# Kernel optimization log

Hardware: AMD Instinct MI355X
Metric: run time of the kernel (lower is better)

Reference implementation:

```python
import jax, jax.numpy as jnp
import numpy as np

B = 1024      # batch
V = 5023      # FLAME vertices
NF = 9976     # FLAME faces
NJ = 5        # joints: global, neck, jaw, eyeL, eyeR
NL = 51       # static landmarks
PARENTS = (-1, 0, 1, 1, 1)


def setup_inputs() -> dict:
    key = jax.random.key(0)
    ks = jax.random.split(key, 16)
    inp = {}
    # trainable flame parameters (small pose magnitudes for realism)
    inp['shape_params'] = jax.random.normal(ks[0], (B, 300), jnp.float32)
    inp['expression_params'] = jax.random.normal(ks[1], (B, 100), jnp.float32)
    inp['global_rot'] = 0.1 * jax.random.normal(ks[2], (B, 3), jnp.float32)
    inp['neck_pose'] = 0.1 * jax.random.normal(ks[3], (B, 3), jnp.float32)
    inp['jaw_pose'] = 0.1 * jax.random.normal(ks[4], (B, 3), jnp.float32)
    inp['eye_pose'] = 0.1 * jax.random.normal(ks[5], (B, 6), jnp.float32)
    inp['transl'] = jax.random.normal(ks[6], (B, 3), jnp.float32)
    # flame buffers
    inp['v_template'] = jax.random.normal(ks[7], (V, 3), jnp.float32)
    inp['shapedirs'] = 0.01 * jax.random.normal(ks[8], (V, 3, 400), jnp.float32)
    inp['posedirs'] = 0.01 * jax.random.normal(ks[9], (36, V * 3), jnp.float32)
    Jreg = jax.random.uniform(ks[10], (NJ, V), jnp.float32)
    inp['J_regressor'] = Jreg / jnp.sum(Jreg, axis=1, keepdims=True)
    W = jax.random.uniform(ks[11], (V, NJ), jnp.float32)
    inp['lbs_weights'] = W / jnp.sum(W, axis=1, keepdims=True)
    bc = jax.random.uniform(ks[12], (NL, 3), jnp.float32)
    inp['lmk_bary_coords'] = bc / jnp.sum(bc, axis=1, keepdims=True)
    inp['parents'] = jnp.array(PARENTS, dtype=jnp.int32)
    inp['faces'] = jax.random.randint(ks[13], (NF, 3), 0, V, jnp.int32)
    inp['lmk_faces_idx'] = jax.random.randint(ks[14], (NL,), 0, NF, jnp.int64)
    return inp


def batch_rodrigues(rvecs):
    # rvecs: [N,3] axis-angle -> [N,3,3] rotation matrices
    angle = jnp.sqrt(jnp.sum(jnp.square(rvecs + 1e-8), axis=1, keepdims=True))  # [N,1]
    axis = rvecs / angle
    s = jnp.sin(angle)[:, :, None]
    c = jnp.cos(angle)[:, :, None]
    rx, ry, rz = axis[:, 0], axis[:, 1], axis[:, 2]
    zeros = jnp.zeros_like(rx)
    K = jnp.stack([zeros, -rz, ry, rz, zeros, -rx, -ry, rx, zeros], axis=1).reshape(-1, 3, 3)
    I = jnp.eye(3, dtype=rvecs.dtype)
    return I + s * K + (1.0 - c) * (K @ K)


def _lbs(betas, full_pose, v_template, shapedirs, posedirs, J_regressor, lbs_weights):
    b = betas.shape[0]
    # shape+expression blendshapes
    v_shaped = v_template[None] + jnp.einsum('bl,vkl->bvk', betas, shapedirs)  # [B,V,3]
    joints = jnp.einsum('jv,bvk->bjk', J_regressor, v_shaped)                 # [B,J,3]
    rot_mats = batch_rodrigues(full_pose.reshape(-1, 3)).reshape(b, NJ, 3, 3)
    # pose blendshapes (exclude root)
    ident = jnp.eye(3, dtype=betas.dtype)
    pose_feature = (rot_mats[:, 1:] - ident).reshape(b, 9 * (NJ - 1))         # [B,36]
    v_posed = v_shaped + (pose_feature @ posedirs).reshape(b, V, 3)
    # rigid kinematic chain
    rel_joints = jnp.concatenate(
        [joints[:, :1], joints[:, 1:] - joints[:, jnp.array(PARENTS[1:])]], axis=1)
    bottom = jnp.broadcast_to(jnp.array([0., 0., 0., 1.], betas.dtype), (b, NJ, 1, 4))
    tf = jnp.concatenate(
        [jnp.concatenate([rot_mats, rel_joints[..., None]], axis=3), bottom], axis=2)  # [B,J,4,4]
    chain = [tf[:, 0]]
    for i in range(1, NJ):
        chain.append(chain[PARENTS[i]] @ tf[:, i])
    transforms = jnp.stack(chain, axis=1)                                    # [B,J,4,4]
    # remove rest-pose joint location from translation column
    jh = jnp.einsum('bjmn,bjn->bjm', transforms[:, :, :3, :3], joints)       # [B,J,3]
    A = transforms.at[:, :, :3, 3].add(-jh)
    # skinning
    T = jnp.einsum('vj,bjmn->bvmn', lbs_weights, A)                          # [B,V,4,4]
    v_h = jnp.concatenate([v_posed, jnp.ones((b, V, 1), betas.dtype)], axis=2)
    verts = jnp.einsum('bvmn,bvn->bvm', T, v_h)[..., :3]                     # [B,V,3]
    return verts, transforms[:, :, :3, 3]


def reference(shape_params, expression_params, global_rot, neck_pose, jaw_pose,
              eye_pose, transl, v_template, shapedirs, posedirs, J_regressor,
              lbs_weights, lmk_bary_coords, parents, faces, lmk_faces_idx):
    betas = jnp.concatenate([shape_params, expression_params], axis=1)       # [B,400]
    full_pose = jnp.concatenate([global_rot, neck_pose, jaw_pose, eye_pose], axis=1)  # [B,15]
    vertices, _ = _lbs(betas, full_pose, v_template, shapedirs, posedirs,
                       J_regressor, lbs_weights)
    # barycentric landmark interpolation
    lmk_faces = faces[lmk_faces_idx]                                         # [L,3]
    lmk_verts = vertices[:, lmk_faces]                                       # [B,L,3,3]
    landmarks_3d = jnp.einsum('blfk,lf->blk', lmk_verts, lmk_bary_coords)    # [B,L,3]
    landmarks_3d = landmarks_3d + transl[:, None]
    vertices = vertices + transl[:, None]
    # default-weights flame regularizer (fixed_shape=None, ref_vertices=None)
    flame_reg = (100.0 * jnp.sum(neck_pose ** 2)
                 + 0.001 * jnp.sum(jaw_pose ** 2)
                 + 0.001 * jnp.sum(shape_params ** 2)
                 + 0.001 * jnp.sum(expression_params ** 2))
    return vertices, landmarks_3d, flame_reg
```

## Files before the change

### kernel.cpp

```cpp
#include <hip/hip_runtime.h>
#include <hip/hip_bf16.h>

#define BATCH 1024
#define NV 5023
#define NJOINT 5
#define NLMK 51
#define N3 (NV*3)
#define NPADB 15072
#define KBETA 400
#define KTOT 448
#define NSTEP 14
#define RB_B (NPADB/16)
#define RB_A 64
#define FRAG 512

#define BM 64
#define BN 48

#define PK_BETA_CH (NPADB*50)
#define PK_BETA_BLKS 2944
#define PK_POSE_CH (RB_B*96)
#define PK_POSE_BLKS 354
#define NVC2 360
#define VCH 14
#define PK_JS_BLKS (3*NVC2)

#define GBM 64
#define GBN 192
#define GNP 79
#define GGRID 1280
#define CH_S 52
#define CH_PAD 4

typedef __attribute__((ext_vector_type(8))) short short8;
typedef __attribute__((ext_vector_type(4))) float floatx4;
typedef __attribute__((ext_vector_type(4))) float float4v;

#define GLDS16(gp, lp) \
    __builtin_amdgcn_global_load_lds( \
        (const __attribute__((address_space(1))) void*)(gp), \
        (__attribute__((address_space(3))) void*)(lp), 16, 0, 0)

#define WS_JS      0
#define WS_BASEJ   24064
#define WS_REG     24512
#define WS_FLAGS   24520
#define WS_AMAT    24576
#define WS_ACT     270336
#define WS_WB      1187840
#define WS_FULL    14692352

__device__ __forceinline__ float ldf(const void* p, long i, int f32) {
    if (f32) return ((const float*)p)[i];
    return __bfloat162float(((const __hip_bfloat16*)p)[i]);
}
__device__ __forceinline__ short8 ld8bf(const void* p, long i, int f32) {
    if (f32) {
        float4v a = *(const float4v*)((const float*)p + i);
        float4v b = *(const float4v*)((const float*)p + i + 4);
        short8 r;
#pragma unroll
        for (int j = 0; j < 4; ++j) {
            __hip_bfloat16 h = __float2bfloat16(a[j]);
            r[j] = *reinterpret_cast<short*>(&h);
        }
#pragma unroll
        for (int j = 0; j < 4; ++j) {
            __hip_bfloat16 h = __float2bfloat16(b[j]);
            r[4 + j] = *reinterpret_cast<short*>(&h);
        }
        return r;
    }
    return *(const short8*)((const __hip_bfloat16*)p + i);
}
__device__ __forceinline__ void stf(void* p, long i, float v, int f32) {
    if (f32) ((float*)p)[i] = v;
    else ((__hip_bfloat16*)p)[i] = __float2bfloat16(v);
}

__device__ __forceinline__ long act2_off(int b, int k) {
    return (((long)(k >> 5) * RB_A + (b >> 4)) * 64 + ((k >> 3) & 3) * 16 + (b & 15)) * 8 + (k & 7);
}

__device__ __forceinline__ int probe_f32(const void* shape_p) {
    int lane = threadIdx.x & 63;
    unsigned short h = ((const unsigned short*)shape_p)[2 * lane];
    union { unsigned short u; __hip_bfloat16 b; } cv; cv.u = h;
    float v = fabsf(__bfloat162float(cv.b));
    if (v != v) v = 3.4e38f;
#pragma unroll
    for (int off = 32; off; off >>= 1) v = fmaxf(v, __shfl_down(v, off));
    v = __shfl(v, 0);
    return v > 1e4f;
}
__device__ __forceinline__ int probe_i64(const void* lmk_idx) {
    int lane = threadIdx.x & 63;
    const int* q = (const int*)lmk_idx;
    int odd_nonzero = (lane < 25) && (q[2*lane + 1] != 0);
    unsigned long long b = __ballot(odd_nonzero);
    return b == 0ull;
}

__global__ void k_init(float* ws0, const void* shape_p, const void* lmk_idx, int* flags) {
    int i = blockIdx.x * 256 + threadIdx.x;
    if (i < 6129) ws0[i] = 0.f;
    if (blockIdx.x == 0 && threadIdx.x < 64) {
        int f = probe_f32(shape_p);
        int i64 = probe_i64(lmk_idx);
        if (threadIdx.x == 0) { flags[0] = f; flags[1] = i64; }
    }
}

__global__ __launch_bounds__(256) void k_prep(const void* __restrict__ shapedirs,
                                              const void* __restrict__ posedirs,
                                              const void* __restrict__ Jreg,
                                              const void* __restrict__ v_template,
                                              const void* __restrict__ shape_p,
                                              float* __restrict__ reg,
                                              float* __restrict__ JS,
                                              float* __restrict__ baseJ,
                                              __hip_bfloat16* __restrict__ Wb,
                                              float* __restrict__ PART) {
    __shared__ float jl[NJOINT * VCH];
    int f32 = probe_f32(shape_p);
    int blk = blockIdx.x, tid = threadIdx.x;
    if (blk < PK_BETA_BLKS) {
        if (blk == 0 && tid == 0) reg[0] = 0.f;
        if (blk < 24) {
            int zi = blk * 256 + tid;
            if (zi < 6000) JS[zi] = 0.f;
            if (zi < 15) baseJ[zi] = 0.f;
        }
        int g = blk * 256 + tid;
        if (g >= PK_BETA_CH) return;
        int n = g / 50, kg = g - n * 50;
        short8 o;
#pragma unroll
        for (int e = 0; e < 8; ++e) o[e] = 0;
        if (n < N3) o = ld8bf(shapedirs, (long)n * KBETA + kg * 8, f32);
        long chunk = ((long)(kg >> 2) * RB_B + (n >> 4)) * 64 + (kg & 3) * 16 + (n & 15);
        *(short8*)(Wb + chunk * 8) = o;
    } else if (blk < PK_BETA_BLKS + PK_POSE_BLKS) {
        int g = (blk - PK_BETA_BLKS) * 256 + tid;
        if (g >= PK_POSE_CH) return;
        int R = g / 96, rem = g - R * 96;
        int c = rem >> 4, fr = rem & 15;
        int n = R * 16 + fr;
        int k0 = KBETA + 8 * c;
        short8 o;
#pragma unroll
        for (int e = 0; e < 8; ++e) o[e] = 0;
        if (n < N3) {
#pragma unroll
            for (int e = 0; e < 8; ++e) {
                int kk = k0 + e - KBETA;
                float val = (kk < 36) ? ldf(posedirs, (long)kk * N3 + n, f32) : 0.f;
                __hip_bfloat16 h = __float2bfloat16(val);
                o[e] = *reinterpret_cast<short*>(&h);
            }
        }
        long chunk = ((long)(k0 >> 5) * RB_B + R) * 64 + ((k0 >> 3) & 3) * 16 + fr;
        *(short8*)(Wb + chunk * 8) = o;
    } else {
        int b2 = blk - (PK_BETA_BLKS + PK_POSE_BLKS);
        int k = b2 / NVC2;
        int vc = b2 - k * NVC2;
        int v0 = vc * VCH;
        if (tid < NJOINT * VCH) {
            int j = tid / VCH, i = tid - j * VCH;
            int v = min(v0 + i, NV - 1);
            jl[tid] = ldf(Jreg, (long)j * NV + v, f32);
        }
        __syncthreads();
        int l2 = tid + 256;
        float acc1[NJOINT] = {0,0,0,0,0};
        float acc2[NJOINT] = {0,0,0,0,0};
#pragma unroll
        for (int i = 0; i < VCH; ++i) {
            int v = v0 + i;
            if (v >= NV) break;
            float s1 = ldf(shapedirs, (long)v*1200 + k*400 + tid, f32);
            float s2 = 0.f;
            if (l2 < 400)       s2 = ldf(shapedirs, (long)v*1200 + k*400 + l2, f32);
            else if (l2 == 400) s2 = ldf(v_template, v*3 + k, f32);
#pragma unroll
            for (int j = 0; j < NJOINT; ++j) {
                float jr = jl[j*VCH + i];
                acc1[j] += jr * s1;
                acc2[j] += jr * s2;
            }
        }
        long base = ((long)(k*NVC2 + vc)*5)*401;
#pragma unroll
        for (int j = 0; j < NJOINT; ++j) {
            PART[base + j*401 + tid] = acc1[j];
            if (l2 <= 400) PART[base + j*401 + l2] = acc2[j];
        }
    }
}

__global__ __launch_bounds__(256) void k_js_red(const float* __restrict__ PART,
                                                float* __restrict__ JS,
                                                float* __restrict__ baseJ) {
    int o = blockIdx.x * 256 + threadIdx.x;
    if (o >= 3*5*401) return;
    int g = blockIdx.y;
    int k = o / 2005, r = o - k*2005;
    int j = r / 401, l = r - j*401;
    float s = 0.f;
    long base = ((long)(k*NVC2 + g*60)*5 + j)*401 + l;
    for (int vc = 0; vc < 60; ++vc) s += PART[base + (long)vc*2005];
    if (l < 400) atomicAdd(&JS[j*1200 + k*400 + l], s);
    else         atomicAdd(&baseJ[j*3 + k], s);
}

__global__ void k_js_atomic(const void* __restrict__ Jreg,
                            const void* __restrict__ shapedirs,
                            const void* __restrict__ v_template,
                            const int* __restrict__ flags,
                            float* __restrict__ JS, float* __restrict__ baseJ) {
    int f32 = flags[0];
    int k = blockIdx.x, vc = blockIdx.y, tid = threadIdx.x;
    int v0 = vc * 79, v1 = min(NV, v0 + 79);
    int l2 = tid + 256;
    float acc1[NJOINT] = {0,0,0,0,0};
    float acc2[NJOINT] = {0,0,0,0,0};
    for (int v = v0; v < v1; ++v) {
        float s1 = ldf(shapedirs, (long)v*1200 + k*400 + tid, f32);
        float s2 = 0.f;
        if (l2 < 400)       s2 = ldf(shapedirs, (long)v*1200 + k*400 + l2, f32);
        else if (l2 == 400) s2 = ldf(v_template, v*3 + k, f32);
#pragma unroll
        for (int j = 0; j < NJOINT; ++j) {
            float jr = ldf(Jreg, j*NV + v, f32);
            acc1[j] += jr * s1;
            acc2[j] += jr * s2;
        }
    }
#pragma unroll
    for (int j = 0; j < NJOINT; ++j) {
        atomicAdd(&JS[j*1200 + k*400 + tid], acc1[j]);
        if (l2 < 400)       atomicAdd(&JS[j*1200 + k*400 + l2], acc2[j]);
        else if (l2 == 400) atomicAdd(&baseJ[j*3 + k], acc2[j]);
    }
}

__global__ __launch_bounds__(64) void k_batch(
        const void* __restrict__ shape_p, const void* __restrict__ expr_p,
        const void* __restrict__ grot, const void* __restrict__ neck,
        const void* __restrict__ jaw,  const void* __restrict__ eye,
        const float* __restrict__ JS, const float* __restrict__ baseJ,
        __hip_bfloat16* __restrict__ Act, float* __restrict__ Amat, float* __restrict__ reg) {
    int f32 = probe_f32(shape_p);
    int b = blockIdx.x, tid = threadIdx.x;
    __shared__ float betas[400];
    __shared__ float Rm[NJOINT][9];
    __shared__ float joints[NJOINT][3];
    __shared__ float Gm[NJOINT][12];

    for (int i = tid; i < 400; i += 64) {
        float v = (i < 300) ? ldf(shape_p, b*300 + i, f32)
                            : ldf(expr_p, b*100 + i - 300, f32);
        betas[i] = v;
        Act[act2_off(b, i)] = __float2bfloat16(v);
    }
    if (tid >= 36 && tid < 48) Act[act2_off(b, 400 + tid)] = __float2bfloat16(0.f);
    __syncthreads();

    if (tid < 60) {
        int o = tid % 15, q = tid / 15;
        int j = o / 3, kk = o - 3*j;
        const float* js = &JS[j*1200 + kk*400 + q*100];
        float s = 0.f;
        for (int l = 0; l < 100; ++l) s += js[l] * betas[q*100 + l];
        s += __shfl_down(s, 15);
        s += __shfl_down(s, 30);
        if (q == 0) joints[j][kk] = s + baseJ[o];
    }
    if (tid < NJOINT) {
        int j = tid;
        float r[3];
        for (int c = 0; c < 3; ++c) {
            if (j == 0)      r[c] = ldf(grot, b*3 + c, f32);
            else if (j == 1) r[c] = ldf(neck, b*3 + c, f32);
            else if (j == 2) r[c] = ldf(jaw,  b*3 + c, f32);
            else if (j == 3) r[c] = ldf(eye,  b*6 + c, f32);
            else             r[c] = ldf(eye,  b*6 + 3 + c, f32);
        }
        float a0 = r[0] + 1e-8f, a1 = r[1] + 1e-8f, a2 = r[2] + 1e-8f;
        float angle = sqrtf(a0*a0 + a1*a1 + a2*a2);
        float inv = 1.0f / angle;
        float rx = r[0]*inv, ry = r[1]*inv, rz = r[2]*inv;
        float s = sinf(angle), c = cosf(angle);
        float K[9] = {0.f, -rz, ry,  rz, 0.f, -rx,  -ry, rx, 0.f};
        float K2[9];
        for (int rr = 0; rr < 3; ++rr)
            for (int cc = 0; cc < 3; ++cc) {
                float t = 0.f;
                for (int m = 0; m < 3; ++m) t += K[rr*3+m] * K[m*3+cc];
                K2[rr*3+cc] = t;
            }
        for (int i2 = 0; i2 < 9; ++i2) {
            float id = (i2 == 0 || i2 == 4 || i2 == 8) ? 1.f : 0.f;
            Rm[j][i2] = id + s*K[i2] + (1.f - c)*K2[i2];
        }
    }
    __syncthreads();

    if (tid < 36) {
        int i = tid / 9 + 1, rc = tid - (tid/9)*9;
        float id = (rc == 0 || rc == 4 || rc == 8) ? 1.f : 0.f;
        Act[act2_off(b, 400 + tid)] = __float2bfloat16(Rm[i][rc] - id);
    }
    if (tid == 0) {
        for (int rr = 0; rr < 3; ++rr) {
            for (int cc = 0; cc < 3; ++cc) Gm[0][rr*4+cc] = Rm[0][rr*3+cc];
            Gm[0][rr*4+3] = joints[0][rr];
        }
        const int par[NJOINT] = {-1, 0, 1, 1, 1};
        for (int j = 1; j < NJOINT; ++j) {
            int p = par[j];
            float rel[3];
            for (int c2 = 0; c2 < 3; ++c2) rel[c2] = joints[j][c2] - joints[p][c2];
            for (int rr = 0; rr < 3; ++rr) {
                for (int cc = 0; cc < 3; ++cc) {
                    float t = 0.f;
                    for (int m = 0; m < 3; ++m) t += Gm[p][rr*4+m] * Rm[j][m*3+cc];
                    Gm[j][rr*4+cc] = t;
                }
                float t = Gm[p][rr*4+3];
                for (int m = 0; m < 3; ++m) t += Gm[p][rr*4+m] * rel[m];
                Gm[j][rr*4+3] = t;
            }
        }
    }
    __syncthreads();

    if (tid < 60) {
        int j = tid / 12, e = tid - j*12, rr = e / 4, cc = e - rr*4;
        float val = Gm[j][e];
        if (cc == 3)
            for (int m = 0; m < 3; ++m) val -= Gm[j][rr*4+m] * joints[j][m];
        Amat[b*60 + tid] = val;
    }

    float part = 0.f;
    for (int i = tid; i < 400; i += 64) part += betas[i]*betas[i];
    part *= 0.001f;
    if (tid == 0) {
        float nn = 0.f, jj = 0.f;
        for (int c = 0; c < 3; ++c) {
            float nv = ldf(neck, b*3+c, f32);
            float jv = ldf(jaw,  b*3+c, f32);
            nn += nv*nv; jj += jv*jv;
        }
        part += 100.f*nn + 0.001f*jj;
    }
    for (int off = 32; off; off >>= 1) part += __shfl_down(part, off);
    if (tid == 0) atomicAdd(reg, part);
}

__global__ __launch_bounds__(512, 2) void k_gemm_lbs_big(
        const __hip_bfloat16* __restrict__ Act,
        const __hip_bfloat16* __restrict__ Wb,
        const void* __restrict__ v_template,
        const float* __restrict__ Amat,
        const void* __restrict__ weights,
        const void* __restrict__ transl,
        const void* __restrict__ shape_p,
        void* __restrict__ out) {
    __shared__ __align__(16) __hip_bfloat16 stage[2][16 * FRAG];
    __shared__ float chunk[8][16 * CH_S + CH_PAD];
    __shared__ float Al[GBM * 60];
    __shared__ float wl[64 * 5];
    __shared__ float tl[GBM * 3];
    __shared__ float vtl[GBN];

    int f32 = probe_f32(shape_p);
    int tid = threadIdx.x;
    int wave = tid >> 6, lane = tid & 63;
    int fr = lane & 15, quad = lane >> 4;
    int mg = wave >> 2, wn = wave & 3;

    int lin = blockIdx.x;
    int xcd = lin & 7, slot = lin >> 3;
    int P = (slot >> 4) * 8 + xcd;
    int mblk = slot & 15;
    if (P >= GNP) return;
    int m0 = mblk * GBM;
    int v0 = P * 64;

    for (int i = tid; i < GBM*60/4; i += 512)
        ((float4v*)Al)[i] = ((const float4v*)(Amat + (long)m0*60))[i];
    if (tid < 320) {
        int v = v0 + tid / 5;
        wl[tid] = (v < NV) ? ldf(weights, v*5 + tid % 5, f32) : 0.f;
    }
    if (tid < GBM*3)
        tl[tid] = ldf(transl, (long)m0*3 + tid, f32);
    if (tid >= 320) {
        int i = tid - 320;
        vtl[i] = ((long)v0*3 + i < N3) ? ldf(v_template, (long)v0*3 + i, f32) : 0.f;
    }

    int r0 = wave*2, r1 = wave*2 + 1;
    long aoff0 = 0, aoff1 = 0;
    const __hip_bfloat16* base0;
    const __hip_bfloat16* base1;
    int sstr0, sstr1;
    {
        if (r0 < 4) { base0 = Act; sstr0 = RB_A; aoff0 = mblk*4 + r0; }
        else {
            long rb = (long)P*12 + (r0 - 4);
            if (rb > RB_B-1) rb = RB_B-1;
            base0 = Wb; sstr0 = RB_B; aoff0 = rb;
        }
        if (r1 < 4) { base1 = Act; sstr1 = RB_A; aoff1 = mblk*4 + r1; }
        else {
            long rb = (long)P*12 + (r1 - 4);
            if (rb > RB_B-1) rb = RB_B-1;
            base1 = Wb; sstr1 = RB_B; aoff1 = rb;
        }
    }
    __hip_bfloat16* lds0[2] = { &stage[0][r0*FRAG], &stage[1][r0*FRAG] };
    __hip_bfloat16* lds1[2] = { &stage[0][r1*FRAG], &stage[1][r1*FRAG] };

    floatx4 acc[2][3];
#pragma unroll
    for (int q = 0; q < 2; ++q)
#pragma unroll
        for (int t = 0; t < 3; ++t) acc[q][t] = (floatx4){0.f,0.f,0.f,0.f};

    asm volatile("s_waitcnt vmcnt(0)" ::: "memory");
    __builtin_amdgcn_sched_barrier(0);
    GLDS16(base0 + ((long)0*sstr0 + aoff0)*FRAG + lane*8, lds0[0]);
    GLDS16(base1 + ((long)0*sstr1 + aoff1)*FRAG + lane*8, lds1[0]);
    GLDS16(base0 + ((long)1*sstr0 + aoff0)*FRAG + lane*8, lds0[1]);
    GLDS16(base1 + ((long)1*sstr1 + aoff1)*FRAG + lane*8, lds1[1]);

#pragma unroll
    for (int s = 0; s < NSTEP; ++s) {
        const int cb = s & 1;
        if (s == NSTEP-1) { asm volatile("s_waitcnt vmcnt(0)" ::: "memory"); }
        else              { asm volatile("s_waitcnt vmcnt(2)" ::: "memory"); }
        __builtin_amdgcn_sched_barrier(0);
        __builtin_amdgcn_s_barrier();
        __builtin_amdgcn_sched_barrier(0);
        const __hip_bfloat16* sb = stage[cb];
        short8 a0 = *(const short8*)&sb[(mg*2 + 0)*FRAG + lane*8];
        short8 a1 = *(const short8*)&sb[(mg*2 + 1)*FRAG + lane*8];
        short8 b0 = *(const short8*)&sb[(4 + wn*3 + 0)*FRAG + lane*8];
        short8 b1 = *(const short8*)&sb[(4 + wn*3 + 1)*FRAG + lane*8];
        short8 b2 = *(const short8*)&sb[(4 + wn*3 + 2)*FRAG + lane*8];
        acc[0][0] = __builtin_amdgcn_mfma_f32_16x16x32_bf16(a0, b0, acc[0][0], 0, 0, 0);
        acc[0][1] = __builtin_amdgcn_mfma_f32_16x16x32_bf16(a0, b1, acc[0][1], 0, 0, 0);
        acc[0][2] = __builtin_amdgcn_mfma_f32_16x16x32_bf16(a0, b2, acc[0][2], 0, 0, 0);
        acc[1][0] = __builtin_amdgcn_mfma_f32_16x16x32_bf16(a1, b0, acc[1][0], 0, 0, 0);
        acc[1][1] = __builtin_amdgcn_mfma_f32_16x16x32_bf16(a1, b1, acc[1][1], 0, 0, 0);
        acc[1][2] = __builtin_amdgcn_mfma_f32_16x16x32_bf16(a1, b2, acc[1][2], 0, 0, 0);
        __builtin_amdgcn_sched_barrier(0);
        __builtin_amdgcn_s_barrier();
        __builtin_amdgcn_sched_barrier(0);
        if (s + 2 < NSTEP) {
            GLDS16(base0 + ((long)(s+2)*sstr0 + aoff0)*FRAG + lane*8, lds0[cb]);
            GLDS16(base1 + ((long)(s+2)*sstr1 + aoff1)*FRAG + lane*8, lds1[cb]);
        }
    }

    __syncthreads();
    float* vbuf = (float*)stage;
    float* ch = chunk[wave];
    int mloc_w = lane;
    float w0 = wl[mloc_w*5+0], w1 = wl[mloc_w*5+1], w2 = wl[mloc_w*5+2];
    float w3 = wl[mloc_w*5+3], w4 = wl[mloc_w*5+4];
    float vt0 = vtl[mloc_w*3+0], vt1 = vtl[mloc_w*3+1], vt2 = vtl[mloc_w*3+2];
    int coff = (mloc_w & 15) * 3;
    int wnl = mloc_w >> 4;
#pragma unroll
    for (int q = 0; q < 2; ++q) {
#pragma unroll
        for (int t = 0; t < 3; ++t)
#pragma unroll
            for (int rr = 0; rr < 4; ++rr)
                ch[(quad*4 + rr)*CH_S + t*16 + fr] = acc[q][t][rr];
        __syncthreads();
        int v = v0 + mloc_w;
#pragma unroll
        for (int it = 0; it < 4; ++it) {
            int r32 = it*8 + wave;
            int mb = ((r32 & 16) << 1) + q*16 + (r32 & 15);
            const float* A = &Al[mb*60];
            const float* cc2 = &chunk[((r32 >> 4) << 2) + wnl][(r32 & 15)*CH_S + coff];
            if (v < NV) {
                float p0 = cc2[0] + vt0;
                float p1 = cc2[1] + vt1;
                float p2 = cc2[2] + vt2;
                float* vb = &vbuf[r32*192 + mloc_w*3];
#pragma unroll
                for (int c = 0; c < 3; ++c) {
                    float t0 = w0*A[c*4+0] + w1*A[12+c*4+0] + w2*A[24+c*4+0] + w3*A[36+c*4+0] + w4*A[48+c*4+0];
                    float t1 = w0*A[c*4+1] + w1*A[12+c*4+1] + w2*A[24+c*4+1] + w3*A[36+c*4+1] + w4*A[48+c*4+1];
                    float t2 = w0*A[c*4+2] + w1*A[12+c*4+2] + w2*A[24+c*4+2] + w3*A[36+c*4+2] + w4*A[48+c*4+2];
                    float t3 = w0*A[c*4+3] + w1*A[12+c*4+3] + w2*A[24+c*4+3] + w3*A[36+c*4+3] + w4*A[48+c*4+3];
                    vb[c] = t0*p0 + t1*p1 + t2*p2 + t3 + tl[mb*3+c];
                }
            }
        }
        __syncthreads();
#pragma unroll
        for (int it = 0; it < 12; ++it) {
            int idx = it*512 + tid;
            int r32 = idx / 192;
            int col = idx - r32*192;
            if (v0*3 + col < N3) {
                int mb = ((r32 & 16) << 1) + q*16 + (r32 & 15);
                stf(out, ((long)(m0 + mb)*NV + v0)*3 + col, vbuf[idx], f32);
            }
        }
        __syncthreads();
    }
}

__global__ __launch_bounds__(256) void k_gemm_lbs_small(
        const __hip_bfloat16* __restrict__ Act,
        const void* __restrict__ shapedirs,
        const void* __restrict__ posedirs,
        const void* __restrict__ v_template,
        const float* __restrict__ Amat,
        const void* __restrict__ weights,
        const void* __restrict__ transl,
        const int* __restrict__ flags,
        void* __restrict__ out) {
    __shared__ float tileS[4][16*49 + 4];
    __shared__ float AlS[4][960];
    __shared__ float wl[80];
    __shared__ __align__(16) __hip_bfloat16 Bs2[BN * 64];

    int f32 = flags[0];
    int tid = threadIdx.x;
    int wave = tid >> 6, lane = tid & 63;
    int fr = lane & 15, quad = lane >> 4;
    int m0 = blockIdx.x * 256;
    int n0 = blockIdx.y * BN;
    int v0 = blockIdx.y * 16;

    if (tid < 80) {
        int v = v0 + tid / 5;
        wl[tid] = (v < NV) ? ldf(weights, v*5 + tid % 5, f32) : 0.f;
    }
    for (int i = tid; i < BN * 64; i += 256) {
        int n = i >> 6, kk = i & 63;
        int nc = min(n0 + n, N3 - 1);
        float val = 0.f;
        if (kk < 16)      val = ldf(shapedirs, (long)nc*KBETA + 384 + kk, f32);
        else if (kk < 52) val = ldf(posedirs, (long)(kk-16)*N3 + nc, f32);
        Bs2[n*64 + kk] = __float2bfloat16(val);
    }
    __syncthreads();

    int Ra0 = (m0 >> 4) + wave*4;
    int nr[3];
#pragma unroll
    for (int t = 0; t < 3; ++t) nr[t] = min(n0 + t*16 + fr, N3 - 1);

    floatx4 acc[4][3];
#pragma unroll
    for (int sub = 0; sub < 4; ++sub)
#pragma unroll
        for (int t = 0; t < 3; ++t) acc[sub][t] = (floatx4){0.f,0.f,0.f,0.f};

#pragma unroll
    for (int s = 0; s < 14; ++s) {
        short8 bb[3];
#pragma unroll
        for (int t = 0; t < 3; ++t) {
            if (s < 12) bb[t] = ld8bf(shapedirs, (long)nr[t]*KBETA + s*32 + quad*8, f32);
            else        bb[t] = *(short8*)&Bs2[(t*16 + fr)*64 + (s-12)*32 + quad*8];
        }
#pragma unroll
        for (int sub = 0; sub < 4; ++sub) {
            short8 a = *(const short8*)(Act + (((long)s*RB_A + Ra0 + sub)*64 + lane)*8);
#pragma unroll
            for (int t = 0; t < 3; ++t)
                acc[sub][t] = __builtin_amdgcn_mfma_f32_16x16x32_bf16(a, bb[t], acc[sub][t], 0, 0, 0);
        }
    }

    int vloc = fr, rgrp = quad;
    int v = v0 + vloc;
    float tpl0 = 0.f, tpl1 = 0.f, tpl2 = 0.f;
    if (v < NV) {
        tpl0 = ldf(v_template, v*3 + 0, f32);
        tpl1 = ldf(v_template, v*3 + 1, f32);
        tpl2 = ldf(v_template, v*3 + 2, f32);
    }
    float w0 = wl[vloc*5+0], w1 = wl[vloc*5+1], w2 = wl[vloc*5+2];
    float w3 = wl[vloc*5+3], w4 = wl[vloc*5+4];
    for (int sub = 0; sub < 4; ++sub) {
#pragma unroll
        for (int t = 0; t < 3; ++t)
#pragma unroll
            for (int rr = 0; rr < 4; ++rr)
                tileS[wave][(quad*4 + rr)*49 + t*16 + fr] = acc[sub][t][rr];
        for (int i = lane; i < 960; i += 64)
            AlS[wave][i] = Amat[(long)(m0 + wave*64 + sub*16)*60 + i];
        __syncthreads();
        if (v < NV) {
#pragma unroll
            for (int rr = 0; rr < 4; ++rr) {
                int mloc = rgrp*4 + rr;
                long m = m0 + wave*64 + sub*16 + mloc;
                float p0 = tileS[wave][mloc*49 + vloc*3 + 0] + tpl0;
                float p1 = tileS[wave][mloc*49 + vloc*3 + 1] + tpl1;
                float p2 = tileS[wave][mloc*49 + vloc*3 + 2] + tpl2;
                const float* A = &AlS[wave][mloc*60];
#pragma unroll
                for (int c = 0; c < 3; ++c) {
                    float t0 = w0*A[c*4+0] + w1*A[12+c*4+0] + w2*A[24+c*4+0] + w3*A[36+c*4+0] + w4*A[48+c*4+0];
                    float t1 = w0*A[c*4+1] + w1*A[12+c*4+1] + w2*A[24+c*4+1] + w3*A[36+c*4+1] + w4*A[48+c*4+1];
                    float t2 = w0*A[c*4+2] + w1*A[12+c*4+2] + w2*A[24+c*4+2] + w3*A[36+c*4+2] + w4*A[48+c*4+2];
                    float t3 = w0*A[c*4+3] + w1*A[12+c*4+3] + w2*A[24+c*4+3] + w3*A[36+c*4+3] + w4*A[48+c*4+3];
                    float val = t0*p0 + t1*p1 + t2*p2 + t3 + ldf(transl, m*3 + c, f32);
                    stf(out, (m*NV + v)*3 + c, val, f32);
                }
            }
        }
        __syncthreads();
    }
}

__global__ __launch_bounds__(64) void k_lmk(const void* __restrict__ verts,
                                            const void* __restrict__ bary,
                                            const int* __restrict__ faces,
                                            const void* __restrict__ lmk_idx,
                                            const void* __restrict__ transl,
                                            const float* __restrict__ reg,
                                            const void* __restrict__ shape_p,
                                            void* __restrict__ out) {
    int f32 = probe_f32(shape_p);
    int i64 = probe_i64(lmk_idx);
    int b = blockIdx.x, tid = threadIdx.x;
    if (b == 0 && tid == 63)
        stf(out, (long)BATCH*NV*3 + (long)BATCH*NLMK*3, reg[0], f32);
    if (tid >= NLMK) return;
    int f = i64 ? (int)((const long long*)lmk_idx)[tid]
                : ((const int*)lmk_idx)[tid];
    float acc[3] = {0.f, 0.f, 0.f};
    float bsum = 0.f;
    for (int fi = 0; fi < 3; ++fi) {
        int vi = faces[f*3 + fi];
        float bc = ldf(bary, tid*3 + fi, f32);
        bsum += bc;
#pragma unroll
        for (int c = 0; c < 3; ++c)
            acc[c] += bc * ldf(verts, ((long)b*NV + vi)*3 + c, f32);
    }
#pragma unroll
    for (int c = 0; c < 3; ++c) {
        float val = acc[c] + (1.f - bsum) * ldf(transl, b*3 + c, f32);
        stf(out, (long)BATCH*NV*3 + ((long)b*NLMK + tid)*3 + c, val, f32);
    }
}

extern "C" void kernel_launch(void* const* d_in, const int* in_sizes, int n_in,
                              void* d_out, int out_size, void* d_ws, size_t ws_size,
                              hipStream_t stream) {
    const void* shape_p   = d_in[0];
    const void* expr_p    = d_in[1];
    const void* grot      = d_in[2];
    const void* neck      = d_in[3];
    const void* jaw       = d_in[4];
    const void* eye       = d_in[5];
    const void* transl    = d_in[6];
    const void* v_templ   = d_in[7];
    const void* shapedirs = d_in[8];
    const void* posedirs  = d_in[9];
    const void* Jreg      = d_in[10];
    const void* weights   = d_in[11];
    const void* bary      = d_in[12];
    const int*  faces     = (const int*)d_in[14];
    const void* lmk_idx   = d_in[15];

    char* ws = (char*)d_ws;
    float* JS      = (float*)(ws + WS_JS);
    float* baseJ   = (float*)(ws + WS_BASEJ);
    float* reg     = (float*)(ws + WS_REG);
    int*   flags   = (int*)(ws + WS_FLAGS);
    float* Amat    = (float*)(ws + WS_AMAT);
    __hip_bfloat16* Act = (__hip_bfloat16*)(ws + WS_ACT);
    __hip_bfloat16* Wb  = (__hip_bfloat16*)(ws + WS_WB);
    float* PART    = (float*)d_out;
    bool big = ws_size >= (size_t)WS_FULL;

    if (big) {
        k_prep<<<PK_BETA_BLKS + PK_POSE_BLKS + PK_JS_BLKS, 256, 0, stream>>>(
            shapedirs, posedirs, Jreg, v_templ, shape_p, reg, JS, baseJ, Wb, PART);
        k_js_red<<<dim3(24, 6), 256, 0, stream>>>(PART, JS, baseJ);
    } else {
        k_init<<<24, 256, 0, stream>>>((float*)ws, shape_p, lmk_idx, flags);
        k_js_atomic<<<dim3(3, 64), 256, 0, stream>>>(Jreg, shapedirs, v_templ, flags, JS, baseJ);
    }
    k_batch<<<BATCH, 64, 0, stream>>>(shape_p, expr_p, grot, neck, jaw, eye,
                                      JS, baseJ, Act, Amat, reg);
    if (big) {
        k_gemm_lbs_big<<<GGRID, 512, 0, stream>>>(Act, Wb, v_templ, Amat,
                                                  weights, transl, shape_p, d_out);
    } else {
        dim3 grid(BATCH/256, (N3 + BN - 1)/BN);
        k_gemm_lbs_small<<<grid, 256, 0, stream>>>(Act, shapedirs, posedirs, v_templ,
                                                   Amat, weights, transl, flags, d_out);
    }
    k_lmk<<<BATCH, 64, 0, stream>>>(d_out, bary, faces, lmk_idx, transl, reg, shape_p, d_out);
}
```

Before: 214.8 us.

## Alias LDS buffers and stage epilogue per sub-pass to raise block occupancy

The MFMA staging buffer, the accumulator chunk buffer and a smaller output staging buffer now share one 32 KB LDS region. This removes the separate chunk array and shrinks the output staging from 32 rows to 8 rows, written and flushed per sub-pass. The LDS footprint drops so more 512-thread blocks can be resident per CU, and launch bounds are raised to 6 blocks per CU. The chunk row stride also changes from 52 to 50 to alter bank mapping. The cost is more barriers in the epilogue and a tighter register budget from the higher launch bound, which could force spills.

```diff
diff --git a/kernel.cpp b/kernel.cpp
--- a/kernel.cpp
+++ b/kernel.cpp
@@ -29,8 +29,9 @@
 #define GBN 192
 #define GNP 79
 #define GGRID 1280
-#define CH_S 52
+#define CH_S 50
 #define CH_PAD 4
+#define CH_W (16*CH_S + CH_PAD)
 
 typedef __attribute__((ext_vector_type(8))) short short8;
 typedef __attribute__((ext_vector_type(4))) float floatx4;
@@ -360,7 +361,7 @@
     if (tid == 0) atomicAdd(reg, part);
 }
 
-__global__ __launch_bounds__(512, 2) void k_gemm_lbs_big(
+__global__ __launch_bounds__(512, 6) void k_gemm_lbs_big(
         const __hip_bfloat16* __restrict__ Act,
         const __hip_bfloat16* __restrict__ Wb,
         const void* __restrict__ v_template,
@@ -369,12 +370,16 @@
         const void* __restrict__ transl,
         const void* __restrict__ shape_p,
         void* __restrict__ out) {
-    __shared__ __align__(16) __hip_bfloat16 stage[2][16 * FRAG];
-    __shared__ float chunk[8][16 * CH_S + CH_PAD];
+    __shared__ __align__(16) char shraw[32768];
     __shared__ float Al[GBM * 60];
     __shared__ float wl[64 * 5];
     __shared__ float tl[GBM * 3];
     __shared__ float vtl[GBN];
+
+    __hip_bfloat16* stageA[2] = { (__hip_bfloat16*)shraw,
+                                  (__hip_bfloat16*)(shraw + 16*FRAG*2) };
+    float* chunkF = (float*)shraw;
+    float* vbuf   = (float*)(shraw + 8*CH_W*4);
 
     int f32 = probe_f32(shape_p);
     int tid = threadIdx.x;
@@ -422,8 +427,8 @@
             base1 = Wb; sstr1 = RB_B; aoff1 = rb;
         }
     }
-    __hip_bfloat16* lds0[2] = { &stage[0][r0*FRAG], &stage[1][r0*FRAG] };
-    __hip_bfloat16* lds1[2] = { &stage[0][r1*FRAG], &stage[1][r1*FRAG] };
+    __hip_bfloat16* lds0[2] = { &stageA[0][r0*FRAG], &stageA[1][r0*FRAG] };
+    __hip_bfloat16* lds1[2] = { &stageA[0][r1*FRAG], &stageA[1][r1*FRAG] };
 
     floatx4 acc[2][3];
 #pragma unroll
@@ -446,7 +451,7 @@
         __builtin_amdgcn_sched_barrier(0);
         __builtin_amdgcn_s_barrier();
         __builtin_amdgcn_sched_barrier(0);
-        const __hip_bfloat16* sb = stage[cb];
+        const __hip_bfloat16* sb = stageA[cb];
         short8 a0 = *(const short8*)&sb[(mg*2 + 0)*FRAG + lane*8];
         short8 a1 = *(const short8*)&sb[(mg*2 + 1)*FRAG + lane*8];
         short8 b0 = *(const short8*)&sb[(4 + wn*3 + 0)*FRAG + lane*8];
@@ -468,14 +473,14 @@
     }
 
     __syncthreads();
-    float* vbuf = (float*)stage;
-    float* ch = chunk[wave];
-    int mloc_w = lane;
-    float w0 = wl[mloc_w*5+0], w1 = wl[mloc_w*5+1], w2 = wl[mloc_w*5+2];
-    float w3 = wl[mloc_w*5+3], w4 = wl[mloc_w*5+4];
-    float vt0 = vtl[mloc_w*3+0], vt1 = vtl[mloc_w*3+1], vt2 = vtl[mloc_w*3+2];
-    int coff = (mloc_w & 15) * 3;
-    int wnl = mloc_w >> 4;
+    float* ch = chunkF + wave*CH_W;
+    int vloc = lane;
+    float w0 = wl[vloc*5+0], w1 = wl[vloc*5+1], w2 = wl[vloc*5+2];
+    float w3 = wl[vloc*5+3], w4 = wl[vloc*5+4];
+    float vt0 = vtl[vloc*3+0], vt1 = vtl[vloc*3+1], vt2 = vtl[vloc*3+2];
+    int coff = (vloc & 15) * 3;
+    int wnl = vloc >> 4;
+    int v = v0 + vloc;
 #pragma unroll
     for (int q = 0; q < 2; ++q) {
 #pragma unroll
@@ -484,18 +489,18 @@
             for (int rr = 0; rr < 4; ++rr)
                 ch[(quad*4 + rr)*CH_S + t*16 + fr] = acc[q][t][rr];
         __syncthreads();
-        int v = v0 + mloc_w;
-#pragma unroll
-        for (int it = 0; it < 4; ++it) {
-            int r32 = it*8 + wave;
+#pragma unroll
+        for (int sp = 0; sp < 4; ++sp) {
+            int r32 = sp*8 + wave;
             int mb = ((r32 & 16) << 1) + q*16 + (r32 & 15);
             const float* A = &Al[mb*60];
-            const float* cc2 = &chunk[((r32 >> 4) << 2) + wnl][(r32 & 15)*CH_S + coff];
+            const float* cc2 = chunkF + (((r32 >> 4) << 2) + wnl)*CH_W
+                                      + (r32 & 15)*CH_S + coff;
             if (v < NV) {
                 float p0 = cc2[0] + vt0;
                 float p1 = cc2[1] + vt1;
                 float p2 = cc2[2] + vt2;
-                float* vb = &vbuf[r32*192 + mloc_w*3];
+                float* vb = &vbuf[wave*192 + vloc*3];
 #pragma unroll
                 for (int c = 0; c < 3; ++c) {
                     float t0 = w0*A[c*4+0] + w1*A[12+c*4+0] + w2*A[24+c*4+0] + w3*A[36+c*4+0] + w4*A[48+c*4+0];
@@ -505,19 +510,20 @@
                     vb[c] = t0*p0 + t1*p1 + t2*p2 + t3 + tl[mb*3+c];
                 }
             }
-        }
-        __syncthreads();
-#pragma unroll
-        for (int it = 0; it < 12; ++it) {
-            int idx = it*512 + tid;
-            int r32 = idx / 192;
-            int col = idx - r32*192;
-            if (v0*3 + col < N3) {
-                int mb = ((r32 & 16) << 1) + q*16 + (r32 & 15);
-                stf(out, ((long)(m0 + mb)*NV + v0)*3 + col, vbuf[idx], f32);
+            __syncthreads();
+#pragma unroll
+            for (int it = 0; it < 3; ++it) {
+                int idx = it*512 + tid;
+                int r8 = idx / 192;
+                int col = idx - r8*192;
+                if (v0*3 + col < N3) {
+                    int r32b = sp*8 + r8;
+                    int mbs = ((r32b & 16) << 1) + q*16 + (r32b & 15);
+                    stf(out, ((long)(m0 + mbs)*NV + v0)*3 + col, vbuf[idx], f32);
+                }
             }
-        }
-        __syncthreads();
+            __syncthreads();
+        }
     }
 }
 
```

Measured after the change: 230.1 us. +7.1%, slower.
